# Kernel optimization log

Measured on AMD Instinct MI355X. Metric: run time of the kernel, lower is better.

The kernel has to match this reference:

```python
import jax, jax.numpy as jnp
import numpy as np

N, E = 100000, 1600000
NFEAT, H2, H3, H4, NCLASS = 512, 256, 256, 128, 16


def setup_inputs() -> dict:
    key = jax.random.key(0)
    ks = jax.random.split(key, 12)
    def glorot(k, shape):
        fan_in = shape[0]
        return jax.random.normal(k, shape, dtype=jnp.float32) * (1.0 / np.sqrt(fan_in))
    return {
        "x": jax.random.normal(ks[0], (N, NFEAT), dtype=jnp.float32),
        "edge_row": jax.random.randint(ks[1], (E,), 0, N, dtype=jnp.int32),
        "edge_col": jax.random.randint(ks[2], (E,), 0, N, dtype=jnp.int32),
        # positive weights ~ normalized adjacency values (scale ~1/avg_degree)
        "edge_val": jax.random.uniform(ks[3], (E,), dtype=jnp.float32) * (1.0 / 16.0),
        "W1": glorot(ks[4], (NFEAT, H2)), "b1": jnp.zeros((H2,), jnp.float32),
        "W2": glorot(ks[5], (H2, H3)),   "b2": jnp.zeros((H3,), jnp.float32),
        "W3": glorot(ks[6], (H3, H4)),   "b3": jnp.zeros((H4,), jnp.float32),
        "Wd": glorot(ks[7], (H4, NCLASS)), "bd": jnp.zeros((NCLASS,), jnp.float32),
    }


def reference(x, edge_row, edge_col, edge_val, W1, b1, W2, b2, W3, b3, Wd, bd):
    n = x.shape[0]

    def spmm(h):
        # adj @ h with adj in COO form: out[row] += val * h[col]
        return jax.ops.segment_sum(edge_val[:, None] * h[edge_col], edge_row, num_segments=n)

    # gc1 -> relu -> (dropout is identity in eval) -> gc2 -> relu -> gc3 -> relu -> dense
    h = jax.nn.relu(spmm(x @ W1) + b1)
    h = jax.nn.relu(spmm(h @ W2) + b2)
    h = jax.nn.relu(spmm(h @ W3) + b3)
    return h @ Wd + bd
```

## Files before the change

kernel.cpp:

```cpp
#include <hip/hip_runtime.h>
#include <hip/hip_bf16.h>
#include <cstdint>
#include <cstddef>

#define NFEAT 512
#define H2 256
#define H3 256
#define H4 128
#define NCLASS 16

typedef __attribute__((ext_vector_type(8))) short short8;
typedef __attribute__((ext_vector_type(4))) float f32x4;
typedef __attribute__((ext_vector_type(4))) unsigned short ushort4v;
typedef __attribute__((ext_vector_type(4))) _Float16 half4v;
typedef __attribute__((ext_vector_type(2))) _Float16 half2v;

#define AS1 __attribute__((address_space(1)))
#define AS3 __attribute__((address_space(3)))

__device__ inline unsigned short f2bf_rne(float x) {
    unsigned int u = __builtin_bit_cast(unsigned int, x);
    unsigned int r = (u + 0x7FFFu + ((u >> 16) & 1u)) >> 16;
    return (unsigned short)r;
}
__device__ inline float bf2f(unsigned short h) {
    return __builtin_bit_cast(float, (unsigned int)h << 16);
}

template <int VM> __device__ __forceinline__ void vm_wait() {
    asm volatile("s_waitcnt vmcnt(%0)" :: "n"(VM) : "memory");
}
__device__ __forceinline__ void lgkm0() {
    asm volatile("s_waitcnt lgkmcnt(0)" ::: "memory");
}

__global__ void k_hist(const int* __restrict__ er, int* __restrict__ cnt, int E) {
    for (int e = blockIdx.x * blockDim.x + threadIdx.x; e < E; e += gridDim.x * blockDim.x)
        atomicAdd(&cnt[er[e]], 1);
}

__global__ void k_scan1(const int* __restrict__ cnt, int* __restrict__ ex,
                        int* __restrict__ bsum, int n) {
    __shared__ int s[256];
    int i = blockIdx.x * 256 + threadIdx.x;
    int v = (i < n) ? cnt[i] : 0;
    s[threadIdx.x] = v;
    __syncthreads();
    #pragma unroll
    for (int off = 1; off < 256; off <<= 1) {
        int t = (threadIdx.x >= (unsigned)off) ? s[threadIdx.x - off] : 0;
        __syncthreads();
        s[threadIdx.x] += t;
        __syncthreads();
    }
    if (i < n) ex[i] = s[threadIdx.x] - v;
    if (threadIdx.x == 255) bsum[blockIdx.x] = s[255];
}

__global__ void k_scan2(int* __restrict__ bsum, int nb) {
    __shared__ int s[512];
    int v = ((int)threadIdx.x < nb) ? bsum[threadIdx.x] : 0;
    s[threadIdx.x] = v;
    __syncthreads();
    #pragma unroll
    for (int off = 1; off < 512; off <<= 1) {
        int t = (threadIdx.x >= (unsigned)off) ? s[threadIdx.x - off] : 0;
        __syncthreads();
        s[threadIdx.x] += t;
        __syncthreads();
    }
    if ((int)threadIdx.x < nb) bsum[threadIdx.x] = s[threadIdx.x] - v;
}

__global__ void k_scan3(int* __restrict__ rp, int* __restrict__ ofs,
                        const int* __restrict__ bsum, const int* __restrict__ cnt,
                        int n) {
    int i = blockIdx.x * 256 + threadIdx.x;
    if (i < n) {
        int v = rp[i] + bsum[blockIdx.x];
        rp[i] = v;
        ofs[i] = v;
        if (i == n - 1) rp[n] = v + cnt[i];
    }
}

__global__ void k_scatter_sl(const int* __restrict__ er, const int* __restrict__ ec,
                             const float* __restrict__ ev, int* __restrict__ ofs,
                             int2* __restrict__ ev2, int E, int sliceSz) {
    const int slice = blockIdx.x & 7;
    const int g = blockIdx.x >> 3;
    const int rlo = slice * sliceSz;
    const int rhi = rlo + sliceSz;
    for (int e = g * 256 + threadIdx.x; e < E; e += 256 * 256) {
        int r = er[e];
        if (r >= rlo && r < rhi) {
            int p = atomicAdd(&ofs[r], 1);
            ev2[p] = make_int2(ec[e], __builtin_bit_cast(int, ev[e]));
        }
    }
}

__global__ __launch_bounds__(256)
void k_packb(const float* __restrict__ W, unsigned short* __restrict__ hi,
             unsigned short* __restrict__ lo, int K, int M) {
    int idx = blockIdx.x * 256 + threadIdx.x;
    int NT = K >> 5;
    int total = (M >> 4) * NT * 64;
    if (idx >= total) return;
    int l = idx & 63;
    int t = (idx >> 6) % NT;
    int cg = idx / (NT << 6);
    int col = cg * 16 + (l & 15);
    int k0 = t * 32 + (l >> 4) * 8;
    short8 h8, l8;
    #pragma unroll
    for (int j = 0; j < 8; ++j) {
        float x = W[(size_t)(k0 + j) * M + col];
        unsigned short h = f2bf_rne(x);
        h8[j] = (short)h;
        l8[j] = (short)f2bf_rne(x - bf2f(h));
    }
    *(short8*)&hi[(size_t)idx * 8] = h8;
    *(short8*)&lo[(size_t)idx * 8] = l8;
}

__global__ __launch_bounds__(256, 3)
void k_gemm1d(const float* __restrict__ X, const unsigned short* __restrict__ Bh,
              const unsigned short* __restrict__ Bl, _Float16* __restrict__ C16, const int N) {
    constexpr int K = 512, M = 256, NT = K / 32;
    __shared__ char smem[40960];
    float* sXf = (float*)smem;
    unsigned short* sAh = (unsigned short*)(smem + 24576);
    unsigned short* sAl = (unsigned short*)(smem + 32768);
    const int tid = threadIdx.x;
    const int lane = tid & 63;
    const int w = tid >> 6;
    const int lm = lane & 15, lk = lane >> 4;
    const int row0 = blockIdx.x * 64;
    const int col0 = w * 64;

    const int kseg = (lane & 7) ^ ((lane >> 3) & 7);
    const int r0 = min(row0 + w * 16 + (lane >> 3), N - 1);
    const int r1 = min(row0 + w * 16 + 8 + (lane >> 3), N - 1);
    const size_t ga0 = (size_t)r0 * K + kseg * 4;
    const size_t ga1 = (size_t)r1 * K + kseg * 4;

    const int crow = w * 16 + (lane >> 2);
    const int ch = lane & 3;
    const int cu0 = ((2 * ch) ^ (crow & 7)) * 4;
    const int cu1 = ((2 * ch + 1) ^ (crow & 7)) * 4;
    const int cwo = crow * 32 + (ch ^ (crow & 3)) * 8;

    const unsigned short* bfh = Bh + ((size_t)(w * 4) * NT) * 512 + lane * 8;
    const unsigned short* bfl = Bl + ((size_t)(w * 4) * NT) * 512 + lane * 8;
    const int aoff = lm * 32 + ((lk ^ (lm & 3)) * 8);

    f32x4 acc[4][4];
    #pragma unroll
    for (int i = 0; i < 4; ++i)
        #pragma unroll
        for (int j = 0; j < 4; ++j) acc[i][j] = (f32x4){0.f, 0.f, 0.f, 0.f};

    auto stage = [&](int bi, int kk) {
        __builtin_amdgcn_global_load_lds((const AS1 void*)(X + ga0 + kk),
                                         (AS3 void*)(sXf + bi * 2048 + w * 512), 16, 0, 0);
        __builtin_amdgcn_global_load_lds((const AS1 void*)(X + ga1 + kk),
                                         (AS3 void*)(sXf + bi * 2048 + w * 512 + 256), 16, 0, 0);
    };

    auto convert = [&](int src, int dst) {
        const float* s = sXf + src * 2048 + crow * 32;
        f32x4 p0 = *(const f32x4*)(s + cu0);
        f32x4 p1 = *(const f32x4*)(s + cu1);
        float vv[8] = {p0.x, p0.y, p0.z, p0.w, p1.x, p1.y, p1.z, p1.w};
        short8 ah, al;
        #pragma unroll
        for (int j = 0; j < 8; ++j) {
            unsigned int uu = __builtin_bit_cast(unsigned int, vv[j]);
            ah[j] = (short)(uu >> 16);
            float hi_ = __builtin_bit_cast(float, uu & 0xFFFF0000u);
            al[j] = (short)f2bf_rne(vv[j] - hi_);
        }
        *(short8*)&sAh[dst * 2048 + cwo] = ah;
        *(short8*)&sAl[dst * 2048 + cwo] = al;
    };

    stage(0, 0); stage(1, 32); stage(2, 64);
    short8 bhf[4], blf[4];
    #pragma unroll
    for (int nf = 0; nf < 4; ++nf) {
        const size_t o = (size_t)nf * NT * 512;
        bhf[nf] = *(const short8*)(bfh + o);
        blf[nf] = *(const short8*)(bfl + o);
    }
    vm_wait<12>();
    convert(0, 0);
    lgkm0();
    __builtin_amdgcn_s_barrier();

    int b0 = 0;

#define G1D_BODY(T, VM)                                                         \
    {                                                                           \
        vm_wait<VM>();                                                          \
        __builtin_amdgcn_s_barrier();                                           \
        __builtin_amdgcn_sched_barrier(0);                                      \
        short8 bhn[4], bln[4];                                                  \
        _Pragma("unroll")                                                       \
        for (int nf = 0; nf < 4; ++nf) { bhn[nf] = bhf[nf]; bln[nf] = blf[nf]; }\
        if ((T) + 1 < NT) {                                                     \
            _Pragma("unroll")                                                   \
            for (int nf = 0; nf < 4; ++nf) {                                    \
                const size_t o = ((size_t)nf * NT + (T) + 1) * 512;             \
                bhn[nf] = *(const short8*)(bfh + o);                            \
                bln[nf] = *(const short8*)(bfl + o);                            \
            }                                                                   \
        }                                                                       \
        __builtin_amdgcn_sched_barrier(0);                                      \
        _Pragma("unroll")                                                       \
        for (int mf = 0; mf < 4; ++mf) {                                        \
            short8 ah = *(const short8*)&sAh[((T) & 1) * 2048 + aoff + mf * 512]; \
            short8 al = *(const short8*)&sAl[((T) & 1) * 2048 + aoff + mf * 512]; \
            _Pragma("unroll")                                                   \
            for (int nf = 0; nf < 4; ++nf) {                                    \
                acc[mf][nf] = __builtin_amdgcn_mfma_f32_16x16x32_bf16(ah, bhf[nf], acc[mf][nf], 0, 0, 0); \
                acc[mf][nf] = __builtin_amdgcn_mfma_f32_16x16x32_bf16(ah, blf[nf], acc[mf][nf], 0, 0, 0); \
                acc[mf][nf] = __builtin_amdgcn_mfma_f32_16x16x32_bf16(al, bhf[nf], acc[mf][nf], 0, 0, 0); \
            }                                                                   \
        }                                                                       \
        if ((T) + 1 < NT) {                                                     \
            int src = b0 + 1; if (src == 3) src = 0;                            \
            convert(src, ((T) + 1) & 1);                                        \
        }                                                                       \
        lgkm0();                                                                \
        __builtin_amdgcn_sched_barrier(0);                                      \
        __builtin_amdgcn_s_barrier();                                           \
        if ((T) + 3 < NT) stage(b0, ((T) + 3) * 32);                            \
        _Pragma("unroll")                                                       \
        for (int nf = 0; nf < 4; ++nf) { bhf[nf] = bhn[nf]; blf[nf] = bln[nf]; }\
        b0 = b0 + 1; if (b0 == 3) b0 = 0;                                       \
    }

    for (int t = 0; t < NT - 2; ++t) G1D_BODY(t, 10);
    G1D_BODY(NT - 2, 8);
    G1D_BODY(NT - 1, 8);
#undef G1D_BODY

    float* sc = (float*)smem;
    #pragma unroll
    for (int mf = 0; mf < 4; ++mf) {
        __syncthreads();
        #pragma unroll
        for (int nf = 0; nf < 4; ++nf)
            #pragma unroll
            for (int r = 0; r < 4; ++r) {
                const int rl = lk * 4 + r;
                const int col = col0 + nf * 16 + lm;
                sc[rl * M + (col ^ (lk << 3))] = acc[mf][nf][r];
            }
        __syncthreads();
        #pragma unroll
        for (int i = 0; i < 4; ++i) {
            const int idx = i * 256 + tid;
            const int rl = idx >> 6, u = idx & 63;
            const int grow = row0 + mf * 16 + rl;
            if (grow < N) {
                f32x4 v = *(const f32x4*)&sc[rl * M + ((u * 4) ^ (((rl >> 2) & 3) << 3))];
                half4v h;
                h[0] = (_Float16)v[0]; h[1] = (_Float16)v[1];
                h[2] = (_Float16)v[2]; h[3] = (_Float16)v[3];
                *(half4v*)&C16[(size_t)grow * M + u * 4] = h;
            }
        }
    }
}

template <int K, int NFW>
__global__ __launch_bounds__(256, 3)
void k_gemm_btc(const unsigned short* __restrict__ Ah, const unsigned short* __restrict__ Al,
                const unsigned short* __restrict__ Bh, const unsigned short* __restrict__ Bl,
                _Float16* __restrict__ C16, const int N) {
    constexpr int M = 64 * NFW;
    constexpr int NT = K / 32;
    constexpr int UPR = 16 * NFW;
    __shared__ char smem[24576];
    unsigned short* sAh = (unsigned short*)smem;
    unsigned short* sAl = sAh + 6144;
    const int tid = threadIdx.x;
    const int lane = tid & 63;
    const int w = tid >> 6;
    const int lm = lane & 15, lk = lane >> 4;
    const int row0 = blockIdx.x * 64;
    const int col0 = w * (16 * NFW);

    const int kseg = (lane & 3) ^ ((lane >> 2) & 3);
    const int gr = min(row0 + w * 16 + (lane >> 2), N - 1);
    const size_t ga = (size_t)gr * K + kseg * 8;

    const int aoff = lm * 32 + ((lk ^ (lm & 3)) * 8);

    const unsigned short* bfh = Bh + ((size_t)(w * NFW) * NT) * 512 + lane * 8;
    const unsigned short* bfl = Bl + ((size_t)(w * NFW) * NT) * 512 + lane * 8;

    f32x4 acc[4][NFW];
    #pragma unroll
    for (int i = 0; i < 4; ++i)
        #pragma unroll
        for (int j = 0; j < NFW; ++j) acc[i][j] = (f32x4){0.f, 0.f, 0.f, 0.f};

    auto stage = [&](int bi, int kk) {
        __builtin_amdgcn_global_load_lds((const AS1 void*)(Ah + ga + kk),
                                         (AS3 void*)(sAh + bi * 2048 + w * 512), 16, 0, 0);
        __builtin_amdgcn_global_load_lds((const AS1 void*)(Al + ga + kk),
                                         (AS3 void*)(sAl + bi * 2048 + w * 512), 16, 0, 0);
    };

    stage(0, 0); stage(1, 32); stage(2, 64);

    short8 bhf[NFW], blf[NFW];
    #pragma unroll
    for (int nf = 0; nf < NFW; ++nf) {
        const size_t o = (size_t)nf * NT * 512;
        bhf[nf] = *(const short8*)(bfh + o);
        blf[nf] = *(const short8*)(bfl + o);
    }

    int bi = 0;

#define GBT_BODY(T, VM)                                                         \
    {                                                                           \
        vm_wait<VM>();                                                          \
        __builtin_amdgcn_s_barrier();                                           \
        __builtin_amdgcn_sched_barrier(0);                                      \
        short8 bhn[NFW], bln[NFW];                                              \
        _Pragma("unroll")                                                       \
        for (int nf = 0; nf < NFW; ++nf) { bhn[nf] = bhf[nf]; bln[nf] = blf[nf]; } \
        if ((T) + 1 < NT) {                                                     \
            _Pragma("unroll")                                                   \
            for (int nf = 0; nf < NFW; ++nf) {                                  \
                const size_t o = ((size_t)nf * NT + (T) + 1) * 512;             \
                bhn[nf] = *(const short8*)(bfh + o);                            \
                bln[nf] = *(const short8*)(bfl + o);                            \
            }                                                                   \
        }                                                                       \
        __builtin_amdgcn_sched_barrier(0);                                      \
        _Pragma("unroll")                                                       \
        for (int mf = 0; mf < 4; ++mf) {                                        \
            short8 ah = *(const short8*)&sAh[bi * 2048 + aoff + mf * 512];      \
            short8 al = *(const short8*)&sAl[bi * 2048 + aoff + mf * 512];      \
            _Pragma("unroll")                                                   \
            for (int nf = 0; nf < NFW; ++nf) {                                  \
                acc[mf][nf] = __builtin_amdgcn_mfma_f32_16x16x32_bf16(ah, bhf[nf], acc[mf][nf], 0, 0, 0); \
                acc[mf][nf] = __builtin_amdgcn_mfma_f32_16x16x32_bf16(ah, blf[nf], acc[mf][nf], 0, 0, 0); \
                acc[mf][nf] = __builtin_amdgcn_mfma_f32_16x16x32_bf16(al, bhf[nf], acc[mf][nf], 0, 0, 0); \
            }                                                                   \
        }                                                                       \
        lgkm0();                                                                \
        __builtin_amdgcn_sched_barrier(0);                                      \
        __builtin_amdgcn_s_barrier();                                           \
        if ((T) + 3 < NT) stage(bi, ((T) + 3) * 32);                            \
        _Pragma("unroll")                                                       \
        for (int nf = 0; nf < NFW; ++nf) { bhf[nf] = bhn[nf]; blf[nf] = bln[nf]; } \
        bi = bi + 1; if (bi == 3) bi = 0;                                       \
    }

    for (int t = 0; t < NT - 2; ++t) GBT_BODY(t, 2 * NFW + 4);
    GBT_BODY(NT - 2, 2 * NFW + 2);
    GBT_BODY(NT - 1, 2 * NFW);
#undef GBT_BODY

    float* sc = (float*)smem;
    #pragma unroll
    for (int mf = 0; mf < 4; ++mf) {
        __syncthreads();
        #pragma unroll
        for (int nf = 0; nf < NFW; ++nf)
            #pragma unroll
            for (int r = 0; r < 4; ++r) {
                const int rl = lk * 4 + r;
                const int col = col0 + nf * 16 + lm;
                sc[rl * M + (col ^ (lk << 3))] = acc[mf][nf][r];
            }
        __syncthreads();
        #pragma unroll
        for (int i = 0; i < (16 * UPR) / 256; ++i) {
            const int idx = i * 256 + tid;
            const int rl = idx / UPR, u = idx % UPR;
            const int grow = row0 + mf * 16 + rl;
            if (grow < N) {
                f32x4 v = *(const f32x4*)&sc[rl * M + ((u * 4) ^ (((rl >> 2) & 3) << 3))];
                half4v h;
                h[0] = (_Float16)v[0]; h[1] = (_Float16)v[1];
                h[2] = (_Float16)v[2]; h[3] = (_Float16)v[3];
                *(half4v*)&C16[(size_t)grow * M + u * 4] = h;
            }
        }
    }
}

__global__ __launch_bounds__(256)
void k_spmm256f(const int* __restrict__ rp, const int2* __restrict__ ev2,
                const _Float16* __restrict__ in16, const float* __restrict__ bias,
                unsigned short* __restrict__ oh, unsigned short* __restrict__ ol, int N) {
    const int lane = threadIdx.x & 63;
    int r = __builtin_amdgcn_readfirstlane(blockIdx.x * 4 + (threadIdx.x >> 6));
    if (r >= N) return;
    const int e0 = __builtin_amdgcn_readfirstlane(rp[r]);
    const int e1 = __builtin_amdgcn_readfirstlane(rp[r + 1]);
    f32x4 acc = {0.f, 0.f, 0.f, 0.f};
    const _Float16* base = in16 + lane * 4;

    #pragma unroll 4
    for (int e = e0; e < e1; ++e) {
        int2 p = ev2[e];
        half4v hv = *(const half4v*)(base + (size_t)p.x * 256);
        float val = __builtin_bit_cast(float, p.y);
        acc[0] = fmaf(val, (float)hv[0], acc[0]);
        acc[1] = fmaf(val, (float)hv[1], acc[1]);
        acc[2] = fmaf(val, (float)hv[2], acc[2]);
        acc[3] = fmaf(val, (float)hv[3], acc[3]);
    }

    f32x4 bv = *(const f32x4*)&bias[lane * 4];
    ushort4v h, l;
    #pragma unroll
    for (int j = 0; j < 4; ++j) {
        float o = fmaxf(acc[j] + bv[j], 0.f);
        unsigned short hh = f2bf_rne(o);
        h[j] = hh;
        l[j] = f2bf_rne(o - bf2f(hh));
    }
    *(ushort4v*)&oh[(size_t)r * 256 + lane * 4] = h;
    *(ushort4v*)&ol[(size_t)r * 256 + lane * 4] = l;
}

__global__ __launch_bounds__(256)
void k_spmm128f(const int* __restrict__ rp, const int2* __restrict__ ev2,
                const _Float16* __restrict__ in16, const float* __restrict__ b3,
                const float* __restrict__ Wd, const float* __restrict__ bd,
                float* __restrict__ out, int N) {
    __shared__ float Ws[H4 * NCLASS];
    __shared__ float hrow[4][H4];
    {
        int i = threadIdx.x * 8;
        *(f32x4*)&Ws[i] = *(const f32x4*)&Wd[i];
        *(f32x4*)&Ws[i + 4] = *(const f32x4*)&Wd[i + 4];
    }
    __syncthreads();

    const int lane = threadIdx.x & 63;
    const int w = threadIdx.x >> 6;
    int r = __builtin_amdgcn_readfirstlane(blockIdx.x * 4 + w);
    if (r >= N) return;
    const int e0 = __builtin_amdgcn_readfirstlane(rp[r]);
    const int e1 = __builtin_amdgcn_readfirstlane(rp[r + 1]);
    float a0 = 0.f, a1 = 0.f;
    const _Float16* base = in16 + lane * 2;

    #pragma unroll 4
    for (int e = e0; e < e1; ++e) {
        int2 p = ev2[e];
        half2v hv = *(const half2v*)(base + (size_t)p.x * 128);
        float v = __builtin_bit_cast(float, p.y);
        a0 = fmaf(v, (float)hv[0], a0);
        a1 = fmaf(v, (float)hv[1], a1);
    }

    float2 hb;
    hb.x = fmaxf(a0 + b3[lane * 2 + 0], 0.f);
    hb.y = fmaxf(a1 + b3[lane * 2 + 1], 0.f);
    *(float2*)&hrow[w][lane * 2] = hb;

    const int c = lane & 15, q = lane >> 4;
    float s = 0.f;
    #pragma unroll
    for (int k = q * 32; k < q * 32 + 32; ++k)
        s = fmaf(hrow[w][k], Ws[k * NCLASS + c], s);
    s += __shfl_xor(s, 16);
    s += __shfl_xor(s, 32);
    if (lane < 16) out[(size_t)r * NCLASS + lane] = s + bd[lane];
}

extern "C" void kernel_launch(void* const* d_in, const int* in_sizes, int n_in,
                              void* d_out, int out_size, void* d_ws, size_t ws_size,
                              hipStream_t stream) {
    const float* x  = (const float*)d_in[0];
    const int*   er = (const int*)d_in[1];
    const int*   ec = (const int*)d_in[2];
    const float* ev = (const float*)d_in[3];
    const float* W1 = (const float*)d_in[4];
    const float* b1 = (const float*)d_in[5];
    const float* W2 = (const float*)d_in[6];
    const float* b2 = (const float*)d_in[7];
    const float* W3 = (const float*)d_in[8];
    const float* b3 = (const float*)d_in[9];
    const float* Wd = (const float*)d_in[10];
    const float* bd = (const float*)d_in[11];
    float* out = (float*)d_out;

    const int N = in_sizes[0] / NFEAT;
    const int E = in_sizes[1];

    char* w = (char*)d_ws;
    auto alloc = [&](size_t bytes) { char* p = w; w += (bytes + 255) & ~(size_t)255; return p; };
    _Float16* C16 = (_Float16*)alloc((size_t)N * 256 * 2);
    unsigned short* hh = (unsigned short*)alloc((size_t)N * 256 * 2);
    unsigned short* hl = (unsigned short*)alloc((size_t)N * 256 * 2);
    int* cnt  = (int*)alloc((size_t)N * 4);
    int* rp   = (int*)alloc((size_t)(N + 1) * 4);
    int* ofs  = (int*)alloc((size_t)N * 4);
    int2* ev2 = (int2*)alloc((size_t)E * 8);
    int* bsum = (int*)alloc(4096);
    unsigned short* W1h = (unsigned short*)alloc((size_t)NFEAT * H2 * 2);
    unsigned short* W1l = (unsigned short*)alloc((size_t)NFEAT * H2 * 2);
    unsigned short* W2h = (unsigned short*)alloc((size_t)H2 * H3 * 2);
    unsigned short* W2l = (unsigned short*)alloc((size_t)H2 * H3 * 2);
    unsigned short* W3h = (unsigned short*)alloc((size_t)H3 * H4 * 2);
    unsigned short* W3l = (unsigned short*)alloc((size_t)H3 * H4 * 2);

    const int nb = (N + 255) / 256;
    const int sliceSz = (N + 7) / 8;

    hipMemsetAsync(cnt, 0, (size_t)N * 4, stream);
    k_hist<<<1024, 256, 0, stream>>>(er, cnt, E);
    k_scan1<<<nb, 256, 0, stream>>>(cnt, rp, bsum, N);
    k_scan2<<<1, 512, 0, stream>>>(bsum, nb);
    k_scan3<<<nb, 256, 0, stream>>>(rp, ofs, bsum, cnt, N);
    k_scatter_sl<<<2048, 256, 0, stream>>>(er, ec, ev, ofs, ev2, E, sliceSz);

    k_packb<<<(NFEAT * H2 / 8 + 255) / 256, 256, 0, stream>>>(W1, W1h, W1l, NFEAT, H2);
    k_packb<<<(H2 * H3 / 8 + 255) / 256, 256, 0, stream>>>(W2, W2h, W2l, H2, H3);
    k_packb<<<(H3 * H4 / 8 + 255) / 256, 256, 0, stream>>>(W3, W3h, W3l, H3, H4);

    const int rgrid = (N + 63) / 64;
    const int sgrid = (N + 3) / 4;

    k_gemm1d<<<rgrid, 256, 0, stream>>>(x, W1h, W1l, C16, N);
    k_spmm256f<<<sgrid, 256, 0, stream>>>(rp, ev2, C16, b1, hh, hl, N);

    k_gemm_btc<H2, 4><<<rgrid, 256, 0, stream>>>(hh, hl, W2h, W2l, C16, N);
    k_spmm256f<<<sgrid, 256, 0, stream>>>(rp, ev2, C16, b2, hh, hl, N);

    k_gemm_btc<H3, 2><<<rgrid, 256, 0, stream>>>(hh, hl, W3h, W3l, C16, N);
    k_spmm128f<<<sgrid, 256, 0, stream>>>(rp, ev2, C16, b3, Wd, bd, out, N);
}
```

Baseline: 656.1 us.

## Store hidden activations as fp16 and split to bf16 hi/lo inside GEMM

```diff
diff --git a/kernel.cpp b/kernel.cpp
--- a/kernel.cpp
+++ b/kernel.cpp
@@ -277,15 +277,16 @@
 
 template <int K, int NFW>
 __global__ __launch_bounds__(256, 3)
-void k_gemm_btc(const unsigned short* __restrict__ Ah, const unsigned short* __restrict__ Al,
-                const unsigned short* __restrict__ Bh, const unsigned short* __restrict__ Bl,
-                _Float16* __restrict__ C16, const int N) {
+void k_gemm_f16a(const _Float16* __restrict__ A16, const unsigned short* __restrict__ Bh,
+                 const unsigned short* __restrict__ Bl, _Float16* __restrict__ Cout,
+                 const int N) {
     constexpr int M = 64 * NFW;
     constexpr int NT = K / 32;
     constexpr int UPR = 16 * NFW;
-    __shared__ char smem[24576];
-    unsigned short* sAh = (unsigned short*)smem;
-    unsigned short* sAl = sAh + 6144;
+    __shared__ char smem[28672];
+    _Float16* sX16 = (_Float16*)smem;
+    unsigned short* sAh = (unsigned short*)(smem + 12288);
+    unsigned short* sAl = (unsigned short*)(smem + 20480);
     const int tid = threadIdx.x;
     const int lane = tid & 63;
     const int w = tid >> 6;
@@ -293,14 +294,17 @@
     const int row0 = blockIdx.x * 64;
     const int col0 = w * (16 * NFW);
 
-    const int kseg = (lane & 3) ^ ((lane >> 2) & 3);
-    const int gr = min(row0 + w * 16 + (lane >> 2), N - 1);
-    const size_t ga = (size_t)gr * K + kseg * 8;
-
-    const int aoff = lm * 32 + ((lk ^ (lm & 3)) * 8);
+    const int grow = min(row0 + w * 16 + (lane >> 2), N - 1);
+    const size_t ga = (size_t)grow * K + (lane & 3) * 8;
+
+    const int crow = w * 16 + (lane >> 2);
+    const int ch = lane & 3;
+    const int cro = (lane >> 2) * 32 + ch * 8;
+    const int cwo = crow * 32 + (ch ^ (crow & 3)) * 8;
 
     const unsigned short* bfh = Bh + ((size_t)(w * NFW) * NT) * 512 + lane * 8;
     const unsigned short* bfl = Bl + ((size_t)(w * NFW) * NT) * 512 + lane * 8;
+    const int aoff = lm * 32 + ((lk ^ (lm & 3)) * 8);
 
     f32x4 acc[4][NFW];
     #pragma unroll
@@ -309,14 +313,27 @@
         for (int j = 0; j < NFW; ++j) acc[i][j] = (f32x4){0.f, 0.f, 0.f, 0.f};
 
     auto stage = [&](int bi, int kk) {
-        __builtin_amdgcn_global_load_lds((const AS1 void*)(Ah + ga + kk),
-                                         (AS3 void*)(sAh + bi * 2048 + w * 512), 16, 0, 0);
-        __builtin_amdgcn_global_load_lds((const AS1 void*)(Al + ga + kk),
-                                         (AS3 void*)(sAl + bi * 2048 + w * 512), 16, 0, 0);
+        __builtin_amdgcn_global_load_lds((const AS1 void*)(A16 + ga + kk),
+                                         (AS3 void*)(sX16 + bi * 2048 + w * 512), 16, 0, 0);
     };
 
+    auto convert = [&](int src, int dst) {
+        short8 raw = *(const short8*)(sX16 + src * 2048 + w * 512 + cro);
+        short8 ah, al;
+        #pragma unroll
+        for (int j = 0; j < 8; ++j) {
+            _Float16 hv = __builtin_bit_cast(_Float16, (unsigned short)raw[j]);
+            float v = (float)hv;
+            unsigned int uu = __builtin_bit_cast(unsigned int, v);
+            ah[j] = (short)(uu >> 16);
+            float hi_ = __builtin_bit_cast(float, uu & 0xFFFF0000u);
+            al[j] = (short)f2bf_rne(v - hi_);
+        }
+        *(short8*)&sAh[dst * 2048 + cwo] = ah;
+        *(short8*)&sAl[dst * 2048 + cwo] = al;
+    };
+
     stage(0, 0); stage(1, 32); stage(2, 64);
-
     short8 bhf[NFW], blf[NFW];
     #pragma unroll
     for (int nf = 0; nf < NFW; ++nf) {
@@ -324,10 +341,14 @@
         bhf[nf] = *(const short8*)(bfh + o);
         blf[nf] = *(const short8*)(bfl + o);
     }
-
-    int bi = 0;
-
-#define GBT_BODY(T, VM)                                                         \
+    vm_wait<2 * NFW + 2>();
+    convert(0, 0);
+    lgkm0();
+    __builtin_amdgcn_s_barrier();
+
+    int b0 = 0;
+
+#define GF_BODY(T, VM)                                                          \
     {                                                                           \
         vm_wait<VM>();                                                          \
         __builtin_amdgcn_s_barrier();                                           \
@@ -346,8 +367,8 @@
         __builtin_amdgcn_sched_barrier(0);                                      \
         _Pragma("unroll")                                                       \
         for (int mf = 0; mf < 4; ++mf) {                                        \
-            short8 ah = *(const short8*)&sAh[bi * 2048 + aoff + mf * 512];      \
-            short8 al = *(const short8*)&sAl[bi * 2048 + aoff + mf * 512];      \
+            short8 ah = *(const short8*)&sAh[((T) & 1) * 2048 + aoff + mf * 512]; \
+            short8 al = *(const short8*)&sAl[((T) & 1) * 2048 + aoff + mf * 512]; \
             _Pragma("unroll")                                                   \
             for (int nf = 0; nf < NFW; ++nf) {                                  \
                 acc[mf][nf] = __builtin_amdgcn_mfma_f32_16x16x32_bf16(ah, bhf[nf], acc[mf][nf], 0, 0, 0); \
@@ -355,19 +376,23 @@
                 acc[mf][nf] = __builtin_amdgcn_mfma_f32_16x16x32_bf16(al, bhf[nf], acc[mf][nf], 0, 0, 0); \
             }                                                                   \
         }                                                                       \
+        if ((T) + 1 < NT) {                                                     \
+            int src = b0 + 1; if (src == 3) src = 0;                            \
+            convert(src, ((T) + 1) & 1);                                        \
+        }                                                                       \
         lgkm0();                                                                \
         __builtin_amdgcn_sched_barrier(0);                                      \
         __builtin_amdgcn_s_barrier();                                           \
-        if ((T) + 3 < NT) stage(bi, ((T) + 3) * 32);                            \
+        if ((T) + 3 < NT) stage(b0, ((T) + 3) * 32);                            \
         _Pragma("unroll")                                                       \
         for (int nf = 0; nf < NFW; ++nf) { bhf[nf] = bhn[nf]; blf[nf] = bln[nf]; } \
-        bi = bi + 1; if (bi == 3) bi = 0;                                       \
-    }
-
-    for (int t = 0; t < NT - 2; ++t) GBT_BODY(t, 2 * NFW + 4);
-    GBT_BODY(NT - 2, 2 * NFW + 2);
-    GBT_BODY(NT - 1, 2 * NFW);
-#undef GBT_BODY
+        b0 = b0 + 1; if (b0 == 3) b0 = 0;                                       \
+    }
+
+    for (int t = 0; t < NT - 2; ++t) GF_BODY(t, 2 * NFW + 1);
+    GF_BODY(NT - 2, 2 * NFW);
+    GF_BODY(NT - 1, 2 * NFW);
+#undef GF_BODY
 
     float* sc = (float*)smem;
     #pragma unroll
@@ -386,13 +411,13 @@
         for (int i = 0; i < (16 * UPR) / 256; ++i) {
             const int idx = i * 256 + tid;
             const int rl = idx / UPR, u = idx % UPR;
-            const int grow = row0 + mf * 16 + rl;
-            if (grow < N) {
+            const int gr2 = row0 + mf * 16 + rl;
+            if (gr2 < N) {
                 f32x4 v = *(const f32x4*)&sc[rl * M + ((u * 4) ^ (((rl >> 2) & 3) << 3))];
                 half4v h;
                 h[0] = (_Float16)v[0]; h[1] = (_Float16)v[1];
                 h[2] = (_Float16)v[2]; h[3] = (_Float16)v[3];
-                *(half4v*)&C16[(size_t)grow * M + u * 4] = h;
+                *(half4v*)&Cout[(size_t)gr2 * M + u * 4] = h;
             }
         }
     }
@@ -401,7 +426,7 @@
 __global__ __launch_bounds__(256)
 void k_spmm256f(const int* __restrict__ rp, const int2* __restrict__ ev2,
                 const _Float16* __restrict__ in16, const float* __restrict__ bias,
-                unsigned short* __restrict__ oh, unsigned short* __restrict__ ol, int N) {
+                _Float16* __restrict__ o16, int N) {
     const int lane = threadIdx.x & 63;
     int r = __builtin_amdgcn_readfirstlane(blockIdx.x * 4 + (threadIdx.x >> 6));
     if (r >= N) return;
@@ -422,16 +447,13 @@
     }
 
     f32x4 bv = *(const f32x4*)&bias[lane * 4];
-    ushort4v h, l;
+    half4v h;
     #pragma unroll
     for (int j = 0; j < 4; ++j) {
         float o = fmaxf(acc[j] + bv[j], 0.f);
-        unsigned short hh = f2bf_rne(o);
-        h[j] = hh;
-        l[j] = f2bf_rne(o - bf2f(hh));
-    }
-    *(ushort4v*)&oh[(size_t)r * 256 + lane * 4] = h;
-    *(ushort4v*)&ol[(size_t)r * 256 + lane * 4] = l;
+        h[j] = (_Float16)o;
+    }
+    *(half4v*)&o16[(size_t)r * 256 + lane * 4] = h;
 }
 
 __global__ __launch_bounds__(256)
@@ -504,8 +526,7 @@
     char* w = (char*)d_ws;
     auto alloc = [&](size_t bytes) { char* p = w; w += (bytes + 255) & ~(size_t)255; return p; };
     _Float16* C16 = (_Float16*)alloc((size_t)N * 256 * 2);
-    unsigned short* hh = (unsigned short*)alloc((size_t)N * 256 * 2);
-    unsigned short* hl = (unsigned short*)alloc((size_t)N * 256 * 2);
+    _Float16* h16 = (_Float16*)alloc((size_t)N * 256 * 2);
     int* cnt  = (int*)alloc((size_t)N * 4);
     int* rp   = (int*)alloc((size_t)(N + 1) * 4);
     int* ofs  = (int*)alloc((size_t)N * 4);
@@ -536,11 +557,11 @@
     const int sgrid = (N + 3) / 4;
 
     k_gemm1d<<<rgrid, 256, 0, stream>>>(x, W1h, W1l, C16, N);
-    k_spmm256f<<<sgrid, 256, 0, stream>>>(rp, ev2, C16, b1, hh, hl, N);
-
-    k_gemm_btc<H2, 4><<<rgrid, 256, 0, stream>>>(hh, hl, W2h, W2l, C16, N);
-    k_spmm256f<<<sgrid, 256, 0, stream>>>(rp, ev2, C16, b2, hh, hl, N);
-
-    k_gemm_btc<H3, 2><<<rgrid, 256, 0, stream>>>(hh, hl, W3h, W3l, C16, N);
+    k_spmm256f<<<sgrid, 256, 0, stream>>>(rp, ev2, C16, b1, h16, N);
+
+    k_gemm_f16a<H2, 4><<<rgrid, 256, 0, stream>>>(h16, W2h, W2l, C16, N);
+    k_spmm256f<<<sgrid, 256, 0, stream>>>(rp, ev2, C16, b2, h16, N);
+
+    k_gemm_f16a<H3, 2><<<rgrid, 256, 0, stream>>>(h16, W3h, W3l, C16, N);
     k_spmm128f<<<sgrid, 256, 0, stream>>>(rp, ev2, C16, b3, Wd, bd, out, N);
 }
```

Result: no change. 650.1 us (-0.9%).
